# Kernel tuning notes

Measured on AMD Instinct MI355X. Metric: run time of the kernel, lower is better.

Reference implementation:

```python
import jax, jax.numpy as jnp
import numpy as np

N_NODES = 100_000
N_EDGES = 1_000_000
D_IN = 128
D_OUT = 64


def setup_inputs() -> dict:
    key = jax.random.key(0)
    k1, k2, k3 = jax.random.split(key, 3)
    x = jax.random.normal(k1, (N_NODES, D_IN), dtype=jnp.float32)
    edge_index = jax.random.randint(k2, (2, N_EDGES), 0, N_NODES)
    W = jax.random.normal(k3, (D_IN, D_OUT), dtype=jnp.float32) / np.float32(np.sqrt(D_IN))
    b = jnp.zeros((D_OUT,), dtype=jnp.float32)
    weight = jnp.float32(0.5)
    temperature = jnp.float32(10.0)
    return {"x": x, "edge_index": edge_index, "weight": weight,
            "temperature": temperature, "W": W, "b": b}


def gcn_conv(x, edge_index, W, b):
    # PyG GCNConv: add self loops, symmetric deg normalization, then aggregate.
    src, dst = edge_index[0], edge_index[1]
    h = x @ W                                                   # [N, D_OUT]
    deg = jnp.ones((N_NODES,), h.dtype).at[dst].add(jnp.ones((src.shape[0],), h.dtype))
    dinv = jax.lax.rsqrt(deg)
    norm = dinv[src] * dinv[dst]                                # [E]
    agg = jax.ops.segment_sum(h[src] * norm[:, None], dst, num_segments=N_NODES)
    # self-loop contribution: norm = deg^-1/2 * deg^-1/2 = 1/deg
    return agg + h * (1.0 / deg)[:, None] + b


def entropy_fn(h, edge_index, temperature):
    # Boltzmann entropy of per-node Dirichlet energies.
    src, dst = edge_index[0], edge_index[1]
    e = jax.ops.segment_sum(jnp.sum((h[dst] - h[src]) ** 2, axis=1),
                            dst, num_segments=N_NODES)          # [N]
    logp = jax.nn.log_softmax(-e / temperature)
    return -jnp.sum(jnp.exp(logp) * logp)


def reference(x, edge_index, weight, temperature, W, b):
    h = gcn_conv(x, edge_index, W, b)
    g = jax.grad(entropy_fn)(h, edge_index, temperature)
    g = g * temperature  # scale_by_temperature=True
    return h + weight * g
```

## Files before the change

kernel.cpp:

```cpp
#include <hip/hip_runtime.h>

#define DIN  128
#define DOUT 64
#define GTN  64
#define BW   512
#define BSH  9
#define EPC  4096
#define NSTATB 400

__global__ __launch_bounds__(256) void k_countboth(const int* __restrict__ src,
                                                   const int* __restrict__ dst,
                                                   unsigned* __restrict__ counts,
                                                   int NBUK, int NC, int E) {
    __shared__ int h0[256], h1[256];
    for (int j = threadIdx.x; j < NBUK; j += 256) { h0[j] = 0; h1[j] = 0; }
    __syncthreads();
    int start = blockIdx.x * EPC;
    int end = min(start + EPC, E);
    for (int i = start + threadIdx.x; i < end; i += 256) {
        atomicAdd(&h0[dst[i] >> BSH], 1);
        atomicAdd(&h1[src[i] >> BSH], 1);
    }
    __syncthreads();
    int M = NBUK * NC;
    for (int j = threadIdx.x; j < NBUK; j += 256) {
        counts[j * NC + blockIdx.x]     = (unsigned)h0[j];
        counts[M + j * NC + blockIdx.x] = (unsigned)h1[j];
    }
}

__global__ __launch_bounds__(256) void k_scanA(const unsigned* __restrict__ data,
                                               unsigned* __restrict__ bsums, int n) {
    __shared__ unsigned s[256];
    int i = blockIdx.x * 256 + threadIdx.x;
    s[threadIdx.x] = (i < n) ? data[i] : 0u;
    __syncthreads();
    for (int st = 128; st > 0; st >>= 1) {
        if (threadIdx.x < st) s[threadIdx.x] += s[threadIdx.x + st];
        __syncthreads();
    }
    if (threadIdx.x == 0) bsums[blockIdx.x] = s[0];
}

__global__ __launch_bounds__(1024) void k_scan2(unsigned* __restrict__ bsums, int NB) {
    __shared__ unsigned s[1024];
    int tid = threadIdx.x;
    unsigned v = (tid < NB) ? bsums[tid] : 0u;
    s[tid] = v;
    __syncthreads();
    for (int st = 1; st < 1024; st <<= 1) {
        unsigned t = (tid >= st) ? s[tid - st] : 0u;
        __syncthreads();
        s[tid] += t;
        __syncthreads();
    }
    if (tid < NB) bsums[tid] = s[tid] - v;
}

__global__ __launch_bounds__(256) void k_scanC(unsigned* __restrict__ data,
                                               const unsigned* __restrict__ bsums, int n) {
    __shared__ unsigned s[256];
    int i = blockIdx.x * 256 + threadIdx.x;
    unsigned v = (i < n) ? data[i] : 0u;
    s[threadIdx.x] = v;
    __syncthreads();
    for (int st = 1; st < 256; st <<= 1) {
        unsigned t = (threadIdx.x >= st) ? s[threadIdx.x - st] : 0u;
        __syncthreads();
        s[threadIdx.x] += t;
        __syncthreads();
    }
    if (i < n) data[i] = s[threadIdx.x] - v + bsums[blockIdx.x];
}

__global__ __launch_bounds__(256) void k_bucket(const int* __restrict__ key,
                                                const int* __restrict__ other,
                                                const unsigned* __restrict__ counts,
                                                int dirOff, unsigned dirBase,
                                                int2* __restrict__ bucketed,
                                                int NBUK, int NC, int E) {
    __shared__ int cur[256];
    for (int j = threadIdx.x; j < NBUK; j += 256)
        cur[j] = (int)(counts[dirOff + j * NC + blockIdx.x] - dirBase);
    __syncthreads();
    int start = blockIdx.x * EPC;
    int end = min(start + EPC, E);
    for (int i = start + threadIdx.x; i < end; i += 256) {
        int k = key[i], o = other[i];
        int pos = atomicAdd(&cur[k >> BSH], 1);
        bucketed[pos] = make_int2(k, o);
    }
}

__global__ __launch_bounds__(256) void k_csr(const int2* __restrict__ bucketed,
                                             const unsigned* __restrict__ counts,
                                             unsigned* __restrict__ off,
                                             int* __restrict__ pay,
                                             unsigned* __restrict__ cnt,
                                             float* __restrict__ dinv,
                                             int dirOff, unsigned dirBase,
                                             int NBUK, int NC, int N, int E) {
    __shared__ int sH[BW];
    __shared__ int sS[2][BW];
    __shared__ int sC[BW];
    int b = blockIdx.x;
    int base = (int)(counts[dirOff + b * NC] - dirBase);
    int end  = (b + 1 < NBUK) ? (int)(counts[dirOff + (b + 1) * NC] - dirBase) : E;

    for (int j = threadIdx.x; j < BW; j += 256) sH[j] = 0;
    __syncthreads();
    for (int i = base + threadIdx.x; i < end; i += 256)
        atomicAdd(&sH[bucketed[i].x & (BW - 1)], 1);
    __syncthreads();
    for (int j = threadIdx.x; j < BW; j += 256) sS[0][j] = sH[j];
    __syncthreads();
    int pin = 0;
    for (int st = 1; st < BW; st <<= 1) {
        for (int j = threadIdx.x; j < BW; j += 256) {
            int v = sS[pin][j];
            if (j >= st) v += sS[pin][j - st];
            sS[pin ^ 1][j] = v;
        }
        __syncthreads();
        pin ^= 1;
    }
    int lo = b * BW;
    for (int j = threadIdx.x; j < BW; j += 256) {
        int excl = j ? sS[pin][j - 1] : 0;
        sC[j] = excl;
        int n = lo + j;
        if (n < N) {
            off[n] = (unsigned)(base + excl);
            if (cnt) {
                cnt[n] = (unsigned)sH[j];
                dinv[n] = rsqrtf((float)sH[j] + 1.f);
            }
        }
    }
    if (threadIdx.x == 0 && b == NBUK - 1) off[N] = (unsigned)E;
    __syncthreads();
    for (int i = base + threadIdx.x; i < end; i += 256) {
        int2 p = bucketed[i];
        int pos = base + atomicAdd(&sC[p.x & (BW - 1)], 1);
        pay[pos] = p.y;
    }
}

__global__ __launch_bounds__(256) void k_gemm(const float* __restrict__ x,
                                              const float* __restrict__ W,
                                              const float* __restrict__ dinv,
                                              float* __restrict__ h0s, int N) {
    __shared__ float Ws[DIN * DOUT];
    for (int i = threadIdx.x; i < DIN * DOUT / 4; i += 256)
        ((float4*)Ws)[i] = ((const float4*)W)[i];

    int tx = threadIdx.x & 15;
    int ty = threadIdx.x >> 4;
    int r0 = blockIdx.x * GTN + ty * 4;
    __syncthreads();
    if (r0 >= N) return;
    const float* xr = x + (size_t)r0 * DIN;

    float acc[4][4] = {};

#define FMA4(aj, w0, w1, w2, w3, j)                                            \
    acc[j][0] = fmaf(aj.x, w0.x, fmaf(aj.y, w1.x, fmaf(aj.z, w2.x, fmaf(aj.w, w3.x, acc[j][0])))); \
    acc[j][1] = fmaf(aj.x, w0.y, fmaf(aj.y, w1.y, fmaf(aj.z, w2.y, fmaf(aj.w, w3.y, acc[j][1])))); \
    acc[j][2] = fmaf(aj.x, w0.z, fmaf(aj.y, w1.z, fmaf(aj.z, w2.z, fmaf(aj.w, w3.z, acc[j][2])))); \
    acc[j][3] = fmaf(aj.x, w0.w, fmaf(aj.y, w1.w, fmaf(aj.z, w2.w, fmaf(aj.w, w3.w, acc[j][3]))));

    if (r0 + 4 <= N) {
        float4 ab[4][4];
#pragma unroll
        for (int s = 0; s < 3; ++s)
#pragma unroll
            for (int j = 0; j < 4; ++j)
                ab[s][j] = *(const float4*)(xr + (size_t)j * DIN + s * 4);
#pragma unroll
        for (int s = 0; s < DIN / 4; ++s) {
            if (s + 3 < DIN / 4) {
#pragma unroll
                for (int j = 0; j < 4; ++j)
                    ab[(s + 3) & 3][j] =
                        *(const float4*)(xr + (size_t)j * DIN + (s + 3) * 4);
            }
            const int k = s * 4;
            float4 w0 = *((float4*)(Ws + (k + 0) * DOUT + 4 * tx));
            float4 w1 = *((float4*)(Ws + (k + 1) * DOUT + 4 * tx));
            float4 w2 = *((float4*)(Ws + (k + 2) * DOUT + 4 * tx));
            float4 w3 = *((float4*)(Ws + (k + 3) * DOUT + 4 * tx));
            FMA4(ab[s & 3][0], w0, w1, w2, w3, 0)
            FMA4(ab[s & 3][1], w0, w1, w2, w3, 1)
            FMA4(ab[s & 3][2], w0, w1, w2, w3, 2)
            FMA4(ab[s & 3][3], w0, w1, w2, w3, 3)
        }
#pragma unroll
        for (int j = 0; j < 4; ++j) {
            int n = r0 + j;
            float dv = dinv[n];
            float4 o = make_float4(acc[j][0] * dv, acc[j][1] * dv,
                                   acc[j][2] * dv, acc[j][3] * dv);
            *((float4*)(h0s + (size_t)n * DOUT + 4 * tx)) = o;
        }
    } else {
        for (int k = 0; k < DIN; k += 4) {
            float4 w0 = *((float4*)(Ws + (k + 0) * DOUT + 4 * tx));
            float4 w1 = *((float4*)(Ws + (k + 1) * DOUT + 4 * tx));
            float4 w2 = *((float4*)(Ws + (k + 2) * DOUT + 4 * tx));
            float4 w3 = *((float4*)(Ws + (k + 3) * DOUT + 4 * tx));
#pragma unroll
            for (int j = 0; j < 4; ++j) {
                if (r0 + j < N) {
                    float4 a = *(const float4*)(xr + (size_t)j * DIN + k);
                    FMA4(a, w0, w1, w2, w3, j)
                }
            }
        }
#pragma unroll
        for (int j = 0; j < 4; ++j) {
            int n = r0 + j;
            if (n < N) {
                float dv = dinv[n];
                float4 o = make_float4(acc[j][0] * dv, acc[j][1] * dv,
                                       acc[j][2] * dv, acc[j][3] * dv);
                *((float4*)(h0s + (size_t)n * DOUT + 4 * tx)) = o;
            }
        }
    }
#undef FMA4
}

__global__ __launch_bounds__(256) void k_agg(const unsigned* __restrict__ off,
                                             const int* __restrict__ pay,
                                             const float* __restrict__ dinv,
                                             const float* __restrict__ h0s,
                                             const float* __restrict__ b,
                                             float* __restrict__ h, int N) {
    int t = threadIdx.x;
    int grp = t >> 4;
    int q = t & 15;
    int n = blockIdx.x * 16 + grp;
    if (n >= N) return;
    unsigned beg = off[n], end = off[n + 1];
    float4 acc = make_float4(0.f, 0.f, 0.f, 0.f);
    for (unsigned base2 = beg; base2 < end; base2 += 16) {
        unsigned idx = base2 + q;
        int pd = (idx < end) ? pay[idx] : 0;
        int jmax = (int)min(16u, end - base2);
        int j = 0;
        for (; j + 8 <= jmax; j += 8) {
            int s0 = __shfl(pd, j + 0, 16);
            int s1 = __shfl(pd, j + 1, 16);
            int s2 = __shfl(pd, j + 2, 16);
            int s3 = __shfl(pd, j + 3, 16);
            int s4 = __shfl(pd, j + 4, 16);
            int s5 = __shfl(pd, j + 5, 16);
            int s6 = __shfl(pd, j + 6, 16);
            int s7 = __shfl(pd, j + 7, 16);
            float4 a0 = *(const float4*)(h0s + (size_t)s0 * DOUT + 4 * q);
            float4 a1 = *(const float4*)(h0s + (size_t)s1 * DOUT + 4 * q);
            float4 a2 = *(const float4*)(h0s + (size_t)s2 * DOUT + 4 * q);
            float4 a3 = *(const float4*)(h0s + (size_t)s3 * DOUT + 4 * q);
            float4 a4 = *(const float4*)(h0s + (size_t)s4 * DOUT + 4 * q);
            float4 a5 = *(const float4*)(h0s + (size_t)s5 * DOUT + 4 * q);
            float4 a6 = *(const float4*)(h0s + (size_t)s6 * DOUT + 4 * q);
            float4 a7 = *(const float4*)(h0s + (size_t)s7 * DOUT + 4 * q);
            acc.x += ((a0.x + a1.x) + (a2.x + a3.x)) + ((a4.x + a5.x) + (a6.x + a7.x));
            acc.y += ((a0.y + a1.y) + (a2.y + a3.y)) + ((a4.y + a5.y) + (a6.y + a7.y));
            acc.z += ((a0.z + a1.z) + (a2.z + a3.z)) + ((a4.z + a5.z) + (a6.z + a7.z));
            acc.w += ((a0.w + a1.w) + (a2.w + a3.w)) + ((a4.w + a5.w) + (a6.w + a7.w));
        }
        for (; j + 4 <= jmax; j += 4) {
            int s0 = __shfl(pd, j + 0, 16);
            int s1 = __shfl(pd, j + 1, 16);
            int s2 = __shfl(pd, j + 2, 16);
            int s3 = __shfl(pd, j + 3, 16);
            float4 a0 = *(const float4*)(h0s + (size_t)s0 * DOUT + 4 * q);
            float4 a1 = *(const float4*)(h0s + (size_t)s1 * DOUT + 4 * q);
            float4 a2 = *(const float4*)(h0s + (size_t)s2 * DOUT + 4 * q);
            float4 a3 = *(const float4*)(h0s + (size_t)s3 * DOUT + 4 * q);
            acc.x += (a0.x + a1.x) + (a2.x + a3.x);
            acc.y += (a0.y + a1.y) + (a2.y + a3.y);
            acc.z += (a0.z + a1.z) + (a2.z + a3.z);
            acc.w += (a0.w + a1.w) + (a2.w + a3.w);
        }
        for (; j < jmax; ++j) {
            int s = __shfl(pd, j, 16);
            float4 a = *(const float4*)(h0s + (size_t)s * DOUT + 4 * q);
            acc.x += a.x; acc.y += a.y; acc.z += a.z; acc.w += a.w;
        }
    }
    float dv = dinv[n];
    float4 hs = *(const float4*)(h0s + (size_t)n * DOUT + 4 * q);
    float4 bv = *(const float4*)(b + 4 * q);
    float4 o;
    o.x = dv * (acc.x + hs.x) + bv.x;
    o.y = dv * (acc.y + hs.y) + bv.y;
    o.z = dv * (acc.z + hs.z) + bv.z;
    o.w = dv * (acc.w + hs.w) + bv.w;
    *(float4*)(h + (size_t)n * DOUT + 4 * q) = o;
}

__global__ __launch_bounds__(256) void k_energy(const unsigned* __restrict__ off,
                                                const int* __restrict__ pay,
                                                const float* __restrict__ h,
                                                float* __restrict__ e,
                                                float* __restrict__ S, int N) {
    int t = threadIdx.x;
    int grp = t >> 4;
    int q = t & 15;
    int n = blockIdx.x * 16 + grp;
    if (n >= N) return;
    unsigned beg = off[n], end = off[n + 1];
    float4 hm = *(const float4*)(h + (size_t)n * DOUT + 4 * q);
    float4 Sa = make_float4(0.f, 0.f, 0.f, 0.f);
    float esum = 0.f;
#define EACC(a)                                                                \
    {                                                                          \
        Sa.x += a.x; Sa.y += a.y; Sa.z += a.z; Sa.w += a.w;                    \
        float dx = hm.x - a.x, dy = hm.y - a.y, dz = hm.z - a.z, dw = hm.w - a.w; \
        esum += dx * dx + dy * dy + dz * dz + dw * dw;                         \
    }
    for (unsigned base2 = beg; base2 < end; base2 += 16) {
        unsigned idx = base2 + q;
        int pd = (idx < end) ? pay[idx] : 0;
        int jmax = (int)min(16u, end - base2);
        int j = 0;
        for (; j + 8 <= jmax; j += 8) {
            int s0 = __shfl(pd, j + 0, 16);
            int s1 = __shfl(pd, j + 1, 16);
            int s2 = __shfl(pd, j + 2, 16);
            int s3 = __shfl(pd, j + 3, 16);
            int s4 = __shfl(pd, j + 4, 16);
            int s5 = __shfl(pd, j + 5, 16);
            int s6 = __shfl(pd, j + 6, 16);
            int s7 = __shfl(pd, j + 7, 16);
            float4 a0 = *(const float4*)(h + (size_t)s0 * DOUT + 4 * q);
            float4 a1 = *(const float4*)(h + (size_t)s1 * DOUT + 4 * q);
            float4 a2 = *(const float4*)(h + (size_t)s2 * DOUT + 4 * q);
            float4 a3 = *(const float4*)(h + (size_t)s3 * DOUT + 4 * q);
            float4 a4 = *(const float4*)(h + (size_t)s4 * DOUT + 4 * q);
            float4 a5 = *(const float4*)(h + (size_t)s5 * DOUT + 4 * q);
            float4 a6 = *(const float4*)(h + (size_t)s6 * DOUT + 4 * q);
            float4 a7 = *(const float4*)(h + (size_t)s7 * DOUT + 4 * q);
            EACC(a0) EACC(a1) EACC(a2) EACC(a3) EACC(a4) EACC(a5) EACC(a6) EACC(a7)
        }
        for (; j + 4 <= jmax; j += 4) {
            int s0 = __shfl(pd, j + 0, 16);
            int s1 = __shfl(pd, j + 1, 16);
            int s2 = __shfl(pd, j + 2, 16);
            int s3 = __shfl(pd, j + 3, 16);
            float4 a0 = *(const float4*)(h + (size_t)s0 * DOUT + 4 * q);
            float4 a1 = *(const float4*)(h + (size_t)s1 * DOUT + 4 * q);
            float4 a2 = *(const float4*)(h + (size_t)s2 * DOUT + 4 * q);
            float4 a3 = *(const float4*)(h + (size_t)s3 * DOUT + 4 * q);
            EACC(a0) EACC(a1) EACC(a2) EACC(a3)
        }
        for (; j < jmax; ++j) {
            int s = __shfl(pd, j, 16);
            float4 a = *(const float4*)(h + (size_t)s * DOUT + 4 * q);
            EACC(a)
        }
    }
#undef EACC
#pragma unroll
    for (int m = 1; m <= 8; m <<= 1) esum += __shfl_xor(esum, m, 16);
    if (q == 0) e[n] = esum;
    *(float4*)(S + (size_t)n * DOUT + 4 * q) = Sa;
}

__global__ __launch_bounds__(256) void k_stats1(const float* __restrict__ e,
                                                const float* __restrict__ Tptr,
                                                float* __restrict__ part, int N) {
    float T = *Tptr;
    float m = -3.4e38f;
    int i0 = blockIdx.x * 256 + threadIdx.x;
    int stride = gridDim.x * 256;
    for (int i = i0; i < N; i += stride) m = fmaxf(m, -e[i] / T);
    __shared__ float sm[256];
    sm[threadIdx.x] = m;
    __syncthreads();
    for (int s = 128; s > 0; s >>= 1) {
        if (threadIdx.x < s) sm[threadIdx.x] = fmaxf(sm[threadIdx.x], sm[threadIdx.x + s]);
        __syncthreads();
    }
    float bm = sm[0];
    __syncthreads();
    float z = 0.f, mm = 0.f;
    for (int i = i0; i < N; i += stride) {
        float t = -e[i] / T - bm;
        float w = __expf(t);
        z += w;
        mm += w * t;
    }
    __shared__ float sz[256], sM[256];
    sz[threadIdx.x] = z;
    sM[threadIdx.x] = mm;
    __syncthreads();
    for (int s = 128; s > 0; s >>= 1) {
        if (threadIdx.x < s) {
            sz[threadIdx.x] += sz[threadIdx.x + s];
            sM[threadIdx.x] += sM[threadIdx.x + s];
        }
        __syncthreads();
    }
    if (threadIdx.x == 0) {
        part[blockIdx.x * 3 + 0] = bm;
        part[blockIdx.x * 3 + 1] = sz[0];
        part[blockIdx.x * 3 + 2] = sM[0];
    }
}

__global__ __launch_bounds__(256) void k_stats2(const float* __restrict__ part,
                                                float* __restrict__ st, int P) {
    __shared__ float sm[256];
    float m = -3.4e38f;
    for (int i = threadIdx.x; i < P; i += 256) m = fmaxf(m, part[3 * i]);
    sm[threadIdx.x] = m;
    __syncthreads();
    for (int s = 128; s > 0; s >>= 1) {
        if (threadIdx.x < s) sm[threadIdx.x] = fmaxf(sm[threadIdx.x], sm[threadIdx.x + s]);
        __syncthreads();
    }
    float gm = sm[0];
    __syncthreads();
    float Z = 0.f, M = 0.f;
    for (int i = threadIdx.x; i < P; i += 256) {
        float mb = part[3 * i], zb = part[3 * i + 1], Mb = part[3 * i + 2];
        float d = mb - gm, eb = __expf(d);
        Z += eb * zb;
        M += eb * (Mb + d * zb);
    }
    __shared__ float sz[256], sM2[256];
    sz[threadIdx.x] = Z;
    sM2[threadIdx.x] = M;
    __syncthreads();
    for (int s = 128; s > 0; s >>= 1) {
        if (threadIdx.x < s) {
            sz[threadIdx.x] += sz[threadIdx.x + s];
            sM2[threadIdx.x] += sM2[threadIdx.x + s];
        }
        __syncthreads();
    }
    if (threadIdx.x == 0) {
        st[0] = gm;
        st[1] = sz[0];
        st[2] = sM2[0];
    }
}

__global__ __launch_bounds__(256) void k_coef(const float* __restrict__ e,
                                              const float* __restrict__ Tptr,
                                              const float* __restrict__ st,
                                              float* __restrict__ c, int N) {
    int n = blockIdx.x * 256 + threadIdx.x;
    if (n >= N) return;
    float T = *Tptr;
    float gm = st[0], Z = st[1], M = st[2];
    float logZ = logf(Z);
    float H = logZ - M / Z;
    float t = -e[n] / T - gm;
    float lp = t - logZ;
    c[n] = expf(lp) * (lp + H);
}

__global__ __launch_bounds__(256) void k_grad_final(const unsigned* __restrict__ off,
                                                    const int* __restrict__ pay,
                                                    const float* __restrict__ c,
                                                    const float* __restrict__ h,
                                                    const float* __restrict__ S,
                                                    const unsigned* __restrict__ cnt,
                                                    const float* __restrict__ wptr,
                                                    float* __restrict__ out, int N) {
    int t = threadIdx.x;
    int grp = t >> 4;
    int q = t & 15;
    int n = blockIdx.x * 16 + grp;
    if (n >= N) return;
    unsigned beg = off[n], end = off[n + 1];
    float A = 0.f;
    float4 B = make_float4(0.f, 0.f, 0.f, 0.f);
    for (unsigned base2 = beg; base2 < end; base2 += 16) {
        unsigned idx = base2 + q;
        int pd = 0;
        float cv = 0.f;
        if (idx < end) {
            pd = pay[idx];
            cv = c[pd];
        }
        int jmax = (int)min(16u, end - base2);
        int j = 0;
        for (; j + 8 <= jmax; j += 8) {
            int s0 = __shfl(pd, j + 0, 16);
            int s1 = __shfl(pd, j + 1, 16);
            int s2 = __shfl(pd, j + 2, 16);
            int s3 = __shfl(pd, j + 3, 16);
            int s4 = __shfl(pd, j + 4, 16);
            int s5 = __shfl(pd, j + 5, 16);
            int s6 = __shfl(pd, j + 6, 16);
            int s7 = __shfl(pd, j + 7, 16);
            float c0 = __shfl(cv, j + 0, 16);
            float c1 = __shfl(cv, j + 1, 16);
            float c2 = __shfl(cv, j + 2, 16);
            float c3 = __shfl(cv, j + 3, 16);
            float c4 = __shfl(cv, j + 4, 16);
            float c5 = __shfl(cv, j + 5, 16);
            float c6 = __shfl(cv, j + 6, 16);
            float c7 = __shfl(cv, j + 7, 16);
            float4 a0 = *(const float4*)(h + (size_t)s0 * DOUT + 4 * q);
            float4 a1 = *(const float4*)(h + (size_t)s1 * DOUT + 4 * q);
            float4 a2 = *(const float4*)(h + (size_t)s2 * DOUT + 4 * q);
            float4 a3 = *(const float4*)(h + (size_t)s3 * DOUT + 4 * q);
            float4 a4 = *(const float4*)(h + (size_t)s4 * DOUT + 4 * q);
            float4 a5 = *(const float4*)(h + (size_t)s5 * DOUT + 4 * q);
            float4 a6 = *(const float4*)(h + (size_t)s6 * DOUT + 4 * q);
            float4 a7 = *(const float4*)(h + (size_t)s7 * DOUT + 4 * q);
            A += ((c0 + c1) + (c2 + c3)) + ((c4 + c5) + (c6 + c7));
            B.x = fmaf(c0, a0.x, fmaf(c1, a1.x, fmaf(c2, a2.x, fmaf(c3, a3.x, B.x))));
            B.x = fmaf(c4, a4.x, fmaf(c5, a5.x, fmaf(c6, a6.x, fmaf(c7, a7.x, B.x))));
            B.y = fmaf(c0, a0.y, fmaf(c1, a1.y, fmaf(c2, a2.y, fmaf(c3, a3.y, B.y))));
            B.y = fmaf(c4, a4.y, fmaf(c5, a5.y, fmaf(c6, a6.y, fmaf(c7, a7.y, B.y))));
            B.z = fmaf(c0, a0.z, fmaf(c1, a1.z, fmaf(c2, a2.z, fmaf(c3, a3.z, B.z))));
            B.z = fmaf(c4, a4.z, fmaf(c5, a5.z, fmaf(c6, a6.z, fmaf(c7, a7.z, B.z))));
            B.w = fmaf(c0, a0.w, fmaf(c1, a1.w, fmaf(c2, a2.w, fmaf(c3, a3.w, B.w))));
            B.w = fmaf(c4, a4.w, fmaf(c5, a5.w, fmaf(c6, a6.w, fmaf(c7, a7.w, B.w))));
        }
        for (; j + 4 <= jmax; j += 4) {
            int s0 = __shfl(pd, j + 0, 16);
            int s1 = __shfl(pd, j + 1, 16);
            int s2 = __shfl(pd, j + 2, 16);
            int s3 = __shfl(pd, j + 3, 16);
            float c0 = __shfl(cv, j + 0, 16);
            float c1 = __shfl(cv, j + 1, 16);
            float c2 = __shfl(cv, j + 2, 16);
            float c3 = __shfl(cv, j + 3, 16);
            float4 a0 = *(const float4*)(h + (size_t)s0 * DOUT + 4 * q);
            float4 a1 = *(const float4*)(h + (size_t)s1 * DOUT + 4 * q);
            float4 a2 = *(const float4*)(h + (size_t)s2 * DOUT + 4 * q);
            float4 a3 = *(const float4*)(h + (size_t)s3 * DOUT + 4 * q);
            A += (c0 + c1) + (c2 + c3);
            B.x = fmaf(c0, a0.x, fmaf(c1, a1.x, fmaf(c2, a2.x, fmaf(c3, a3.x, B.x))));
            B.y = fmaf(c0, a0.y, fmaf(c1, a1.y, fmaf(c2, a2.y, fmaf(c3, a3.y, B.y))));
            B.z = fmaf(c0, a0.z, fmaf(c1, a1.z, fmaf(c2, a2.z, fmaf(c3, a3.z, B.z))));
            B.w = fmaf(c0, a0.w, fmaf(c1, a1.w, fmaf(c2, a2.w, fmaf(c3, a3.w, B.w))));
        }
        for (; j < jmax; ++j) {
            int s = __shfl(pd, j, 16);
            float cj = __shfl(cv, j, 16);
            float4 a = *(const float4*)(h + (size_t)s * DOUT + 4 * q);
            A += cj;
            B.x = fmaf(cj, a.x, B.x);
            B.y = fmaf(cj, a.y, B.y);
            B.z = fmaf(cj, a.z, B.z);
            B.w = fmaf(cj, a.w, B.w);
        }
    }
    size_t idx4 = (size_t)n * DOUT + 4 * q;
    float4 hm = *(const float4*)(h + idx4);
    float4 Sv = *(const float4*)(S + idx4);
    float cn = c[n];
    float cc = (float)cnt[n];
    float w = *wptr;
    float4 o;
    o.x = hm.x + w * (2.f * cn * (cc * hm.x - Sv.x) + 2.f * (A * hm.x - B.x));
    o.y = hm.y + w * (2.f * cn * (cc * hm.y - Sv.y) + 2.f * (A * hm.y - B.y));
    o.z = hm.z + w * (2.f * cn * (cc * hm.z - Sv.z) + 2.f * (A * hm.z - B.z));
    o.w = hm.w + w * (2.f * cn * (cc * hm.w - Sv.w) + 2.f * (A * hm.w - B.w));
    *(float4*)(out + idx4) = o;
}

extern "C" void kernel_launch(void* const* d_in, const int* in_sizes, int n_in,
                              void* d_out, int out_size, void* d_ws, size_t ws_size,
                              hipStream_t stream) {
    const float* x    = (const float*)d_in[0];
    const int*   ei   = (const int*)d_in[1];
    const float* wptr = (const float*)d_in[2];
    const float* Tptr = (const float*)d_in[3];
    const float* W    = (const float*)d_in[4];
    const float* b    = (const float*)d_in[5];
    float* out = (float*)d_out;

    const int N  = in_sizes[0] / DIN;
    const int E  = in_sizes[1] / 2;
    const int NE = N * DOUT;
    const int* src = ei;
    const int* dst = ei + E;

    const int NBUK = (N + BW - 1) / BW;
    const int NC   = (E + EPC - 1) / EPC;
    const int M    = NBUK * NC;
    const int M2   = 2 * M;
    const int NBs  = (M2 + 255) / 256;

    float*    h0s  = (float*)d_ws;
    float*    h    = h0s + NE;
    int2*     bkt  = (int2*)(h + NE);
    int*      pay1 = (int*)(bkt + E);
    int*      pay2 = pay1 + E;
    unsigned* counts = (unsigned*)(pay2 + E);
    unsigned* bsum = counts + M2;
    unsigned* off1 = bsum + 1024;
    unsigned* off2 = off1 + N + 1;
    unsigned* cnt  = off2 + N + 1;
    float*    e    = (float*)(cnt + N);
    float*    c    = e + N;
    float*    dinv = c + N;
    float*    part = dinv + N;
    float*    st   = part + 3 * NSTATB;
    float*    S    = h0s;

    const int nodeG = (N + 15) / 16;
    const int nodeBlocks = (N + 255) / 256;

    k_countboth<<<NC, 256, 0, stream>>>(src, dst, counts, NBUK, NC, E);
    k_scanA<<<NBs, 256, 0, stream>>>(counts, bsum, M2);
    k_scan2<<<1, 1024, 0, stream>>>(bsum, NBs);
    k_scanC<<<NBs, 256, 0, stream>>>(counts, bsum, M2);

    k_bucket<<<NC, 256, 0, stream>>>(dst, src, counts, 0, 0u, bkt, NBUK, NC, E);
    k_csr<<<NBUK, 256, 0, stream>>>(bkt, counts, off1, pay1, cnt, dinv,
                                    0, 0u, NBUK, NC, N, E);
    k_bucket<<<NC, 256, 0, stream>>>(src, dst, counts, M, (unsigned)E, bkt, NBUK, NC, E);
    k_csr<<<NBUK, 256, 0, stream>>>(bkt, counts, off2, pay2, nullptr, nullptr,
                                    M, (unsigned)E, NBUK, NC, N, E);

    k_gemm<<<(N + GTN - 1) / GTN, 256, 0, stream>>>(x, W, dinv, h0s, N);
    k_agg<<<nodeG, 256, 0, stream>>>(off1, pay1, dinv, h0s, b, h, N);
    k_energy<<<nodeG, 256, 0, stream>>>(off1, pay1, h, e, S, N);
    k_stats1<<<NSTATB, 256, 0, stream>>>(e, Tptr, part, N);
    k_stats2<<<1, 256, 0, stream>>>(part, st, NSTATB);
    k_coef<<<nodeBlocks, 256, 0, stream>>>(e, Tptr, st, c, N);
    k_grad_final<<<nodeG, 256, 0, stream>>>(off2, pay2, c, h, S, cnt, wptr, out, N);
}
```

Baseline: 330.3 us.

## Rewrite GEMM as one row per thread with uniform W loads

The x@W kernel no longer stages W in shared memory with a 4x4 register tile per thread. Each thread now computes a full 64-wide output row, keeping 64 accumulators in registers. W is read directly from global memory at addresses that are the same across the wavefront, so the compiler may turn these into scalar loads. This drops LDS traffic and the block barrier, but x rows are now read with a per-thread stride of 512 bytes, which gives poorly coalesced loads, and register pressure rises.

```diff
diff --git a/kernel.cpp b/kernel.cpp
--- a/kernel.cpp
+++ b/kernel.cpp
@@ -2,7 +2,6 @@
 
 #define DIN  128
 #define DOUT 64
-#define GTN  64
 #define BW   512
 #define BSH  9
 #define EPC  4096
@@ -146,88 +145,52 @@
     }
 }
 
-__global__ __launch_bounds__(256) void k_gemm(const float* __restrict__ x,
-                                              const float* __restrict__ W,
-                                              const float* __restrict__ dinv,
-                                              float* __restrict__ h0s, int N) {
-    __shared__ float Ws[DIN * DOUT];
-    for (int i = threadIdx.x; i < DIN * DOUT / 4; i += 256)
-        ((float4*)Ws)[i] = ((const float4*)W)[i];
-
-    int tx = threadIdx.x & 15;
-    int ty = threadIdx.x >> 4;
-    int r0 = blockIdx.x * GTN + ty * 4;
-    __syncthreads();
-    if (r0 >= N) return;
-    const float* xr = x + (size_t)r0 * DIN;
-
-    float acc[4][4] = {};
-
-#define FMA4(aj, w0, w1, w2, w3, j)                                            \
-    acc[j][0] = fmaf(aj.x, w0.x, fmaf(aj.y, w1.x, fmaf(aj.z, w2.x, fmaf(aj.w, w3.x, acc[j][0])))); \
-    acc[j][1] = fmaf(aj.x, w0.y, fmaf(aj.y, w1.y, fmaf(aj.z, w2.y, fmaf(aj.w, w3.y, acc[j][1])))); \
-    acc[j][2] = fmaf(aj.x, w0.z, fmaf(aj.y, w1.z, fmaf(aj.z, w2.z, fmaf(aj.w, w3.z, acc[j][2])))); \
-    acc[j][3] = fmaf(aj.x, w0.w, fmaf(aj.y, w1.w, fmaf(aj.z, w2.w, fmaf(aj.w, w3.w, acc[j][3]))));
-
-    if (r0 + 4 <= N) {
-        float4 ab[4][4];
-#pragma unroll
-        for (int s = 0; s < 3; ++s)
-#pragma unroll
-            for (int j = 0; j < 4; ++j)
-                ab[s][j] = *(const float4*)(xr + (size_t)j * DIN + s * 4);
-#pragma unroll
-        for (int s = 0; s < DIN / 4; ++s) {
-            if (s + 3 < DIN / 4) {
-#pragma unroll
-                for (int j = 0; j < 4; ++j)
-                    ab[(s + 3) & 3][j] =
-                        *(const float4*)(xr + (size_t)j * DIN + (s + 3) * 4);
+__global__ __launch_bounds__(64) void k_gemm(const float* __restrict__ x,
+                                             const float* __restrict__ W,
+                                             const float* __restrict__ dinv,
+                                             float* __restrict__ h0s, int N) {
+    int row = blockIdx.x * 64 + threadIdx.x;
+    int rc = min(row, N - 1);
+    const float* xr = x + (size_t)rc * DIN;
+
+    float acc[DOUT];
+#pragma unroll
+    for (int c = 0; c < DOUT; ++c) acc[c] = 0.f;
+
+#pragma unroll
+    for (int kc = 0; kc < DIN; kc += 32) {
+        float4 xa[8];
+#pragma unroll
+        for (int j = 0; j < 8; ++j)
+            xa[j] = *(const float4*)(xr + kc + 4 * j);
+#pragma unroll
+        for (int j = 0; j < 8; ++j) {
+            const float* Wb = W + (size_t)(kc + 4 * j) * DOUT;
+            float4 a = xa[j];
+#pragma unroll
+            for (int c4 = 0; c4 < 16; ++c4) {
+                float4 w0 = *(const float4*)(Wb + 0 * DOUT + 4 * c4);
+                float4 w1 = *(const float4*)(Wb + 1 * DOUT + 4 * c4);
+                float4 w2 = *(const float4*)(Wb + 2 * DOUT + 4 * c4);
+                float4 w3 = *(const float4*)(Wb + 3 * DOUT + 4 * c4);
+                acc[4 * c4 + 0] = fmaf(a.x, w0.x, fmaf(a.y, w1.x, fmaf(a.z, w2.x, fmaf(a.w, w3.x, acc[4 * c4 + 0]))));
+                acc[4 * c4 + 1] = fmaf(a.x, w0.y, fmaf(a.y, w1.y, fmaf(a.z, w2.y, fmaf(a.w, w3.y, acc[4 * c4 + 1]))));
+                acc[4 * c4 + 2] = fmaf(a.x, w0.z, fmaf(a.y, w1.z, fmaf(a.z, w2.z, fmaf(a.w, w3.z, acc[4 * c4 + 2]))));
+                acc[4 * c4 + 3] = fmaf(a.x, w0.w, fmaf(a.y, w1.w, fmaf(a.z, w2.w, fmaf(a.w, w3.w, acc[4 * c4 + 3]))));
             }
-            const int k = s * 4;
-            float4 w0 = *((float4*)(Ws + (k + 0) * DOUT + 4 * tx));
-            float4 w1 = *((float4*)(Ws + (k + 1) * DOUT + 4 * tx));
-            float4 w2 = *((float4*)(Ws + (k + 2) * DOUT + 4 * tx));
-            float4 w3 = *((float4*)(Ws + (k + 3) * DOUT + 4 * tx));
-            FMA4(ab[s & 3][0], w0, w1, w2, w3, 0)
-            FMA4(ab[s & 3][1], w0, w1, w2, w3, 1)
-            FMA4(ab[s & 3][2], w0, w1, w2, w3, 2)
-            FMA4(ab[s & 3][3], w0, w1, w2, w3, 3)
-        }
-#pragma unroll
-        for (int j = 0; j < 4; ++j) {
-            int n = r0 + j;
-            float dv = dinv[n];
-            float4 o = make_float4(acc[j][0] * dv, acc[j][1] * dv,
-                                   acc[j][2] * dv, acc[j][3] * dv);
-            *((float4*)(h0s + (size_t)n * DOUT + 4 * tx)) = o;
-        }
-    } else {
-        for (int k = 0; k < DIN; k += 4) {
-            float4 w0 = *((float4*)(Ws + (k + 0) * DOUT + 4 * tx));
-            float4 w1 = *((float4*)(Ws + (k + 1) * DOUT + 4 * tx));
-            float4 w2 = *((float4*)(Ws + (k + 2) * DOUT + 4 * tx));
-            float4 w3 = *((float4*)(Ws + (k + 3) * DOUT + 4 * tx));
-#pragma unroll
-            for (int j = 0; j < 4; ++j) {
-                if (r0 + j < N) {
-                    float4 a = *(const float4*)(xr + (size_t)j * DIN + k);
-                    FMA4(a, w0, w1, w2, w3, j)
-                }
-            }
-        }
-#pragma unroll
-        for (int j = 0; j < 4; ++j) {
-            int n = r0 + j;
-            if (n < N) {
-                float dv = dinv[n];
-                float4 o = make_float4(acc[j][0] * dv, acc[j][1] * dv,
-                                       acc[j][2] * dv, acc[j][3] * dv);
-                *((float4*)(h0s + (size_t)n * DOUT + 4 * tx)) = o;
-            }
-        }
-    }
-#undef FMA4
+        }
+    }
+
+    if (row < N) {
+        float dv = dinv[row];
+        float* o = h0s + (size_t)row * DOUT;
+#pragma unroll
+        for (int c4 = 0; c4 < 16; ++c4) {
+            float4 v = make_float4(acc[4 * c4 + 0] * dv, acc[4 * c4 + 1] * dv,
+                                   acc[4 * c4 + 2] * dv, acc[4 * c4 + 3] * dv);
+            *(float4*)(o + 4 * c4) = v;
+        }
+    }
 }
 
 __global__ __launch_bounds__(256) void k_agg(const unsigned* __restrict__ off,
@@ -624,7 +587,7 @@
     k_csr<<<NBUK, 256, 0, stream>>>(bkt, counts, off2, pay2, nullptr, nullptr,
                                     M, (unsigned)E, NBUK, NC, N, E);
 
-    k_gemm<<<(N + GTN - 1) / GTN, 256, 0, stream>>>(x, W, dinv, h0s, N);
+    k_gemm<<<(N + 63) / 64, 64, 0, stream>>>(x, W, dinv, h0s, N);
     k_agg<<<nodeG, 256, 0, stream>>>(off1, pay1, dinv, h0s, b, h, N);
     k_energy<<<nodeG, 256, 0, stream>>>(off1, pay1, h, e, S, N);
     k_stats1<<<NSTATB, 256, 0, stream>>>(e, Tptr, part, N);
```

Measured after the change: 355.9 us. 7.7% more time.
